# Optimization experiments

Hardware: AMD Instinct MI355X
Metric: run time of the kernel (lower is better)

## Reference

```python
import jax, jax.numpy as jnp
import numpy as np

B, S, E, H = 4, 2048, 1024, 16
HD = E // H  # head_dim = 64


def setup_inputs() -> dict:
    key = jax.random.key(0)
    k1, k2, k3, k4 = jax.random.split(key, 4)
    x = jax.random.normal(k1, (B, S, E), dtype=jnp.float32)
    Wqkv = jax.random.normal(k2, (3 * E, E), dtype=jnp.float32) * (E ** -0.5)
    Wo = jax.random.normal(k3, (E, E), dtype=jnp.float32) * (E ** -0.5)
    bo = jax.random.normal(k4, (E,), dtype=jnp.float32) * 0.01
    return {"x": x, "Wqkv": Wqkv, "Wo": Wo, "bo": bo}


def reference(x, Wqkv, Wo, bo):
    b, s, e = x.shape
    # qkv projection (nn.Linear without bias: x @ W^T) -> (b, s, 3e)
    qkv = x @ Wqkv.T
    # reshape (b, s, H, 3*HD) -> (b, H, s, 3*HD), then chunk into q,k,v
    qkv = qkv.reshape(b, s, H, 3 * HD).transpose(0, 2, 1, 3)
    q, k, v = jnp.split(qkv, 3, axis=-1)  # each (b, H, s, HD)
    scale = 1.0 / jnp.sqrt(jnp.asarray(HD, dtype=x.dtype))
    scores = jnp.einsum('bhqd,bhkd->bhqk', q, k) * scale  # (b, H, s, s)
    causal = jnp.tril(jnp.ones((s, s), dtype=bool))
    scores = jnp.where(causal, scores, -jnp.inf)
    probs = jax.nn.softmax(scores, axis=-1)
    out = jnp.einsum('bhqk,bhkd->bhqd', probs, v)  # (b, H, s, HD)
    out = out.transpose(0, 2, 1, 3).reshape(b, s, e)
    return out @ Wo.T + bo
```

## Files before the change

kernel.cpp:

```cpp
#include <hip/hip_runtime.h>
#include <stdint.h>

#define Bn 4
#define Sn 2048
#define En 1024
#define Hn 16
#define HDn 64

typedef __bf16 bf16;
typedef __bf16 bf16x4 __attribute__((ext_vector_type(4)));
typedef __bf16 bf16x8 __attribute__((ext_vector_type(8)));
typedef float  f32x4  __attribute__((ext_vector_type(4)));
typedef float  f32x16 __attribute__((ext_vector_type(16)));
typedef uint32_t u32x4 __attribute__((ext_vector_type(4)));

#define GLDS(gp, lp) __builtin_amdgcn_global_load_lds( \
    (const __attribute__((address_space(1))) void*)(gp), \
    (__attribute__((address_space(3))) void*)(lp), 16, 0, 0)

#define BAR() __builtin_amdgcn_s_barrier()
#define WLG() do { asm volatile("s_waitcnt lgkmcnt(0)" ::: "memory"); \
                   __builtin_amdgcn_sched_barrier(0); } while (0)
#define WVM4() asm volatile("s_waitcnt vmcnt(4)" ::: "memory")
#define WVM0() asm volatile("s_waitcnt vmcnt(0)" ::: "memory")

__global__ __launch_bounds__(256) void cvt_f32_to_bf16(
    const float* __restrict__ in, bf16* __restrict__ out, int n4)
{
    int i = blockIdx.x * 256 + threadIdx.x;
    if (i >= n4) return;
    float4 f = reinterpret_cast<const float4*>(in)[i];
    bf16x4 o;
    o[0] = (bf16)f.x; o[1] = (bf16)f.y; o[2] = (bf16)f.z; o[3] = (bf16)f.w;
    reinterpret_cast<bf16x4*>(out)[i] = o;
}

template<int MODE>
__global__ __launch_bounds__(512, 2) void gemm256(
    const bf16* __restrict__ Ag, const bf16* __restrict__ Bw,
    int M, int N, int K,
    bf16* __restrict__ q_out, bf16* __restrict__ k_out, bf16* __restrict__ v_out,
    float* __restrict__ c_out, const float* __restrict__ bias)
{
    __shared__ __align__(16) bf16 lA[2 * 256 * 64];
    __shared__ __align__(16) bf16 lB[2 * 256 * 64];

    const int tid  = threadIdx.x;
    const int lane = tid & 63;
    const int w    = tid >> 6;
    const int wm = w >> 2, wn = w & 3;
    const int lr = lane & 15, lg = lane >> 4;
    const int m0 = blockIdx.y * 256;
    const int n0 = blockIdx.x * 256;
    const int NT = K >> 6;
    const int niter = NT >> 1;

    const int srow = tid >> 3;
    const int sck  = (tid & 7) ^ ((tid >> 3) & 7);

    f32x4 acc[8][4] = {};

    auto stageA = [&](int t, int half) {
        const int ts = t < NT ? t : NT - 1;
        bf16* Ld = lA + ((t & 1) ? 16384 : 0) + (half*128 + w*8) * 64;
        const bf16* S = Ag + (size_t)(m0 + half*128 + srow) * K + ts*64 + sck*8;
        GLDS(S, Ld);
        GLDS(S + (size_t)64 * K, Ld + 64 * 64);
    };
    auto stageB = [&](int t, int half) {
        const int ts = t < NT ? t : NT - 1;
        bf16* Ld = lB + ((t & 1) ? 16384 : 0) + (half*128 + w*8) * 64;
        const bf16* S = Bw + (size_t)(n0 + half*128 + srow) * K + ts*64 + sck*8;
        GLDS(S, Ld);
        GLDS(S + (size_t)64 * K, Ld + 64 * 64);
    };
    auto ldA4 = [&](bf16x8 (&a)[4][2], const bf16* Lb, int qm) {
        #pragma unroll
        for (int ii = 0; ii < 4; ++ii) {
            const bf16* p = Lb + (wm*128 + qm*64 + ii*16 + lr) * 64;
            #pragma unroll
            for (int kk = 0; kk < 2; ++kk)
                a[ii][kk] = *reinterpret_cast<const bf16x8*>(p + (((kk << 2) + lg) ^ (lr & 7)) * 8);
        }
    };
    auto ldB2 = [&](bf16x8 (&b)[2][2], const bf16* Lb, int qn) {
        #pragma unroll
        for (int j = 0; j < 2; ++j) {
            const bf16* p = Lb + (wn*64 + qn*32 + j*16 + lr) * 64;
            #pragma unroll
            for (int kk = 0; kk < 2; ++kk)
                b[j][kk] = *reinterpret_cast<const bf16x8*>(p + (((kk << 2) + lg) ^ (lr & 7)) * 8);
        }
    };
    auto mmac = [&](const bf16x8 (&a)[4][2], const bf16x8 (&b)[2][2], int qm, int qn) {
        __builtin_amdgcn_s_setprio(1);
        #pragma unroll
        for (int ii = 0; ii < 4; ++ii)
            #pragma unroll
            for (int j = 0; j < 2; ++j)
                #pragma unroll
                for (int kk = 0; kk < 2; ++kk)
                    acc[qm*4 + ii][qn*2 + j] = __builtin_amdgcn_mfma_f32_16x16x32_bf16(
                        a[ii][kk], b[j][kk], acc[qm*4 + ii][qn*2 + j], 0, 0, 0);
        __builtin_amdgcn_s_setprio(0);
    };

    stageA(0, 0); stageA(0, 1); stageB(0, 0); stageB(0, 1);
    stageB(1, 0); stageB(1, 1);
    WVM4(); BAR();

    const bf16* A0 = lA;          const bf16* A1 = lA + 16384;
    const bf16* B0l = lB;         const bf16* B1l = lB + 16384;
    bf16x8 a[4][2], b0[2][2], b1[2][2];

    for (int i = 0; i < niter; ++i) {
        const int t = 2 * i;
        ldA4(a, A0, 0); ldB2(b0, B0l, 0);
        stageA(t + 1, 0);
        BAR(); WLG();
        mmac(a, b0, 0, 0);
        BAR();
        ldB2(b1, B0l, 1);
        stageA(t + 1, 1);
        BAR(); WLG();
        mmac(a, b1, 0, 1);
        BAR();
        ldA4(a, A0, 1);
        stageB(t + 2, 0);
        BAR(); WLG();
        mmac(a, b0, 1, 0);
        BAR();
        stageB(t + 2, 1);
        WVM4(); BAR();
        mmac(a, b1, 1, 1);
        BAR();
        ldA4(a, A1, 0); ldB2(b0, B1l, 0);
        stageA(t + 2, 0);
        BAR(); WLG();
        mmac(a, b0, 0, 0);
        BAR();
        ldB2(b1, B1l, 1);
        stageA(t + 2, 1);
        BAR(); WLG();
        mmac(a, b1, 0, 1);
        BAR();
        ldA4(a, A1, 1);
        stageB(t + 3, 0);
        BAR(); WLG();
        mmac(a, b0, 1, 0);
        BAR();
        stageB(t + 3, 1);
        WVM4(); BAR();
        mmac(a, b1, 1, 1);
        BAR();
    }

    #pragma unroll
    for (int ii = 0; ii < 8; ++ii) {
        #pragma unroll
        for (int j = 0; j < 4; ++j) {
            const int colb = n0 + wn*64 + j*16 + lr;
            #pragma unroll
            for (int r = 0; r < 4; ++r) {
                const int rowb = m0 + wm*128 + ii*16 + lg*4 + r;
                const float v = acc[ii][j][r];
                if (MODE == 0) {
                    const int bb = rowb >> 11, s = rowb & (Sn - 1);
                    const int h = colb / 192, rr = colb - h*192;
                    const int wq = rr >> 6, hd = rr & 63;
                    const size_t off = (((size_t)(bb*Hn + h))*Sn + s)*HDn + hd;
                    const bf16 bv = (bf16)v;
                    if (wq == 0)      q_out[off] = bv;
                    else if (wq == 1) k_out[off] = bv;
                    else              v_out[off] = bv;
                } else {
                    c_out[(size_t)rowb*N + colb] = v + bias[colb];
                }
            }
        }
    }
}

template<int MODE>
__global__ __launch_bounds__(256) void gemm_bt(
    const bf16* __restrict__ A, const bf16* __restrict__ Bw,
    int M, int N, int K,
    bf16* __restrict__ q_out, bf16* __restrict__ k_out, bf16* __restrict__ v_out,
    float* __restrict__ c_out, const float* __restrict__ bias)
{
    __shared__ bf16 lA[128*64];
    __shared__ bf16 lB[128*64];
    const int tid  = threadIdx.x;
    const int lane = tid & 63;
    const int wv   = tid >> 6;
    const int wm = wv >> 1, wn = wv & 1;
    const int m0 = blockIdx.y * 128;
    const int n0 = blockIdx.x * 128;
    const int lr = lane & 15, lg = lane >> 4;

    f32x4 acc[4][4] = {};

    const int rowA = wv*8 + (lane>>3);
    const int col8 = (lane&7)*8;

    for (int k0 = 0; k0 < K; k0 += 64) {
        #pragma unroll
        for (int c = 0; c < 4; ++c) {
            int row = c*32 + rowA;
            GLDS(A  + (size_t)(m0+row)*K + k0 + col8, lA + (c*32 + wv*8)*64);
            GLDS(Bw + (size_t)(n0+row)*K + k0 + col8, lB + (c*32 + wv*8)*64);
        }
        __syncthreads();
        #pragma unroll
        for (int kk = 0; kk < 64; kk += 32) {
            bf16x8 af[4], bfv[4];
            #pragma unroll
            for (int i = 0; i < 4; ++i)
                af[i] = *reinterpret_cast<const bf16x8*>(lA + (wm*64 + i*16 + lr)*64 + kk + lg*8);
            #pragma unroll
            for (int j = 0; j < 4; ++j)
                bfv[j] = *reinterpret_cast<const bf16x8*>(lB + (wn*64 + j*16 + lr)*64 + kk + lg*8);
            #pragma unroll
            for (int i = 0; i < 4; ++i)
                #pragma unroll
                for (int j = 0; j < 4; ++j)
                    acc[i][j] = __builtin_amdgcn_mfma_f32_16x16x32_bf16(af[i], bfv[j], acc[i][j], 0, 0, 0);
        }
        __syncthreads();
    }

    #pragma unroll
    for (int i = 0; i < 4; ++i) {
        #pragma unroll
        for (int j = 0; j < 4; ++j) {
            const int colb = n0 + wn*64 + j*16 + lr;
            #pragma unroll
            for (int r = 0; r < 4; ++r) {
                const int rowb = m0 + wm*64 + i*16 + lg*4 + r;
                const float v = acc[i][j][r];
                if (MODE == 0) {
                    const int b = rowb >> 11, s = rowb & (Sn-1);
                    const int h = colb / 192, rr = colb - h*192;
                    const int wq = rr >> 6, hd = rr & 63;
                    const size_t off = (((size_t)(b*Hn + h))*Sn + s)*HDn + hd;
                    const bf16 bv = (bf16)v;
                    if (wq == 0)      q_out[off] = bv;
                    else if (wq == 1) k_out[off] = bv;
                    else              v_out[off] = bv;
                } else {
                    c_out[(size_t)rowb*N + colb] = v + bias[colb];
                }
            }
        }
    }
}

static __device__ __forceinline__ uint32_t pkbf(float lo, float hi)
{
    uint16_t a = __builtin_bit_cast(uint16_t, (bf16)lo);
    uint16_t b = __builtin_bit_cast(uint16_t, (bf16)hi);
    return (uint32_t)a | ((uint32_t)b << 16);
}

__global__ __launch_bounds__(512) void attn_fwd(
    const bf16* __restrict__ Q, const bf16* __restrict__ Kg, const bf16* __restrict__ Vg,
    bf16* __restrict__ O)
{
    __shared__ __align__(16) bf16 Kl[2][64*64];
    __shared__ __align__(16) bf16 Vt[2][64*64];

    const int tid  = threadIdx.x;
    const int lane = tid & 63;
    const int w    = tid >> 6;
    const int col  = lane & 31;
    const int hv   = lane >> 5;
    const int bh   = blockIdx.x;
    const int qb   = (gridDim.y - 1) - blockIdx.y;
    const int q0w  = qb*256 + w*32;
    const int qg   = q0w + col;

    const bf16* Qb = Q  + (size_t)bh*Sn*HDn;
    const bf16* Kb = Kg + (size_t)bh*Sn*HDn;
    const bf16* Vb = Vg + (size_t)bh*Sn*HDn;

    bf16x8 aq[4];
    #pragma unroll
    for (int ks = 0; ks < 4; ++ks)
        aq[ks] = *reinterpret_cast<const bf16x8*>(Qb + (size_t)qg*HDn + ks*16 + hv*8);

    f32x16 ov[2] = {};
    const float S2 = 0.18033688011112042f;
    float m_run = -1e30f, l_run = 0.f;

    const int srow = tid >> 3;
    const int scol = tid & 7;
    const int ksw  = scol ^ (srow & 7);

    auto vWrite = [&](bf16* Vd, bf16x8 vv) {
        #pragma unroll
        for (int j = 0; j < 8; ++j) {
            const int chunk = (scol*8 + j)*8 + ((srow>>3) ^ scol);
            Vd[chunk*8 + (srow&7)] = vv[j];
        }
    };

    const int nkt = 4*(qb+1);

    GLDS(Kb + (size_t)srow*HDn + ksw*8, &Kl[0][0] + (size_t)w*512);
    {
        bf16x8 vv0 = *reinterpret_cast<const bf16x8*>(Vb + (size_t)srow*HDn + scol*8);
        WVM0();
        vWrite(&Vt[0][0], vv0);
    }
    __syncthreads();

    for (int kt = 0; kt < nkt; ++kt) {
        const int cur = kt & 1;
        const int k0 = kt*64;
        const bool more = (kt + 1 < nkt);
        const bool skip = (k0 > q0w + 31);

        bf16x8 vv;
        if (more) {
            GLDS(Kb + (size_t)(k0 + 64 + srow)*HDn + ksw*8, &Kl[cur^1][0] + (size_t)w*512);
            vv = *reinterpret_cast<const bf16x8*>(Vb + (size_t)(k0 + 64 + srow)*HDn + scol*8);
        }

        uint32_t wpk[2][8];
        if (!skip) {
            f32x16 st[2] = {};
            __builtin_amdgcn_s_setprio(1);
            #pragma unroll
            for (int kb = 0; kb < 2; ++kb) {
                const int key = kb*32 + col;
                #pragma unroll
                for (int ks = 0; ks < 4; ++ks) {
                    const int chunk = key*8 + ((ks*2 + hv) ^ (key & 7));
                    bf16x8 kf = *reinterpret_cast<const bf16x8*>(&Kl[cur][0] + chunk*8);
                    st[kb] = __builtin_amdgcn_mfma_f32_32x32x16_bf16(kf, aq[ks], st[kb], 0, 0, 0);
                }
            }
            __builtin_amdgcn_s_setprio(0);

            if (k0 + 63 > q0w) {
                #pragma unroll
                for (int kb = 0; kb < 2; ++kb)
                    #pragma unroll
                    for (int r = 0; r < 16; ++r) {
                        const int keyg = k0 + kb*32 + (r&3) + 8*(r>>2) + 4*hv;
                        if (keyg > qg) st[kb][r] = -1e30f;
                    }
            }

            float mx = st[0][0];
            #pragma unroll
            for (int kb = 0; kb < 2; ++kb)
                #pragma unroll
                for (int r = 0; r < 16; ++r)
                    mx = fmaxf(mx, st[kb][r]);
            mx = fmaxf(mx, __shfl_xor(mx, 32));
            const float smax2 = mx * S2;

            if (!__all(smax2 - m_run <= 8.0f)) {
                const float mn = fmaxf(m_run, smax2);
                const float fr = exp2f(m_run - mn);
                l_run *= fr;
                #pragma unroll
                for (int hb = 0; hb < 2; ++hb)
                    #pragma unroll
                    for (int r = 0; r < 16; ++r)
                        ov[hb][r] *= fr;
                m_run = mn;
            }

            float sum = 0.f;
            #pragma unroll
            for (int kb = 0; kb < 2; ++kb)
                #pragma unroll
                for (int i = 0; i < 8; ++i) {
                    const float e0 = exp2f(fmaf(st[kb][2*i],   S2, -m_run));
                    const float e1 = exp2f(fmaf(st[kb][2*i+1], S2, -m_run));
                    sum += e0 + e1;
                    wpk[kb][i] = pkbf(e0, e1);
                }
            l_run += sum;
        }

        WVM0();
        if (more) vWrite(&Vt[cur^1][0], vv);

        if (!skip) {
            #pragma unroll
            for (int s = 0; s < 4; ++s) {
                const int kb = s >> 1, ls = s & 1;
                const uint32_t send0 = hv ? wpk[kb][4*ls+0] : wpk[kb][4*ls+2];
                const uint32_t send1 = hv ? wpk[kb][4*ls+1] : wpk[kb][4*ls+3];
                const uint32_t keep0 = hv ? wpk[kb][4*ls+2] : wpk[kb][4*ls+0];
                const uint32_t keep1 = hv ? wpk[kb][4*ls+3] : wpk[kb][4*ls+1];
                const uint32_t r0 = (uint32_t)__shfl_xor((int)send0, 32);
                const uint32_t r1 = (uint32_t)__shfl_xor((int)send1, 32);
                u32x4 pwv = { hv ? r0 : keep0, hv ? r1 : keep1,
                              hv ? keep0 : r0, hv ? keep1 : r1 };
                bf16x8 pB = __builtin_bit_cast(bf16x8, pwv);
                __builtin_amdgcn_s_setprio(1);
                #pragma unroll
                for (int hb = 0; hb < 2; ++hb) {
                    const int hd = hb*32 + col;
                    const int chunk = hd*8 + ((s*2 + hv) ^ ((hd>>3) & 7));
                    bf16x8 vf = *reinterpret_cast<const bf16x8*>(&Vt[cur][0] + chunk*8);
                    ov[hb] = __builtin_amdgcn_mfma_f32_32x32x16_bf16(vf, pB, ov[hb], 0, 0, 0);
                }
                __builtin_amdgcn_s_setprio(0);
            }
        }

        __syncthreads();
    }

    const float lt  = l_run + __shfl_xor(l_run, 32);
    const float inv = 1.0f / lt;
    const int b = bh >> 4, hh = bh & 15;
    bf16* Ob = O + ((size_t)(b*Sn + qg))*En + hh*HDn;
    #pragma unroll
    for (int hb = 0; hb < 2; ++hb)
        #pragma unroll
        for (int g = 0; g < 4; ++g) {
            bf16x4 o4;
            #pragma unroll
            for (int r4 = 0; r4 < 4; ++r4)
                o4[r4] = (bf16)(ov[hb][g*4 + r4] * inv);
            *reinterpret_cast<bf16x4*>(Ob + hb*32 + g*8 + 4*hv) = o4;
        }
}

extern "C" void kernel_launch(void* const* d_in, const int* in_sizes, int n_in,
                              void* d_out, int out_size, void* d_ws, size_t ws_size,
                              hipStream_t stream)
{
    (void)in_sizes; (void)n_in; (void)out_size; (void)ws_size;
    const float* x    = (const float*)d_in[0];
    const float* Wqkv = (const float*)d_in[1];
    const float* Wo   = (const float*)d_in[2];
    const float* bo   = (const float*)d_in[3];
    float* out = (float*)d_out;

    const size_t nBS = (size_t)Bn*Sn;
    char* ws = (char*)d_ws;
    bf16* xb    = (bf16*)ws; ws += nBS*En*2;
    bf16* wqkvb = (bf16*)ws; ws += (size_t)3*En*En*2;
    bf16* wob   = (bf16*)ws; ws += (size_t)En*En*2;
    bf16* Qb    = (bf16*)ws; ws += nBS*En*2;
    bf16* Kb    = (bf16*)ws; ws += nBS*En*2;
    bf16* Vb    = (bf16*)ws; ws += nBS*En*2;
    bf16* AO    = (bf16*)ws; ws += nBS*En*2;

    int n4 = (int)(nBS*En/4);
    cvt_f32_to_bf16<<<(n4+255)/256, 256, 0, stream>>>(x, xb, n4);
    n4 = 3*En*En/4;
    cvt_f32_to_bf16<<<(n4+255)/256, 256, 0, stream>>>(Wqkv, wqkvb, n4);
    n4 = En*En/4;
    cvt_f32_to_bf16<<<(n4+255)/256, 256, 0, stream>>>(Wo, wob, n4);

    gemm256<0><<<dim3(3*En/256, nBS/256), 512, 0, stream>>>(
        xb, wqkvb, (int)nBS, 3*En, En, Qb, Kb, Vb, nullptr, nullptr);

    attn_fwd<<<dim3(Bn*Hn, Sn/256), 512, 0, stream>>>(Qb, Kb, Vb, AO);

    gemm_bt<1><<<dim3(En/128, nBS/128), 256, 0, stream>>>(
        AO, wob, (int)nBS, En, En, nullptr, nullptr, nullptr, out, bo);
}
```

Before: 204.3 us.

## Prefetch K/V tiles into registers and store to LDS after compute

The attention kernel now loads the next K tile through registers instead of global_load_lds, and writes both the K and V prefetches into the other LDS buffer only after the QK^T, softmax and PV work for the current tile. This moves the vmcnt wait to the end of the iteration so global load latency overlaps the whole compute phase. The max and sum reductions are also rewritten as trees to shorten the dependency chains. The MODE 0 epilogue is removed from gemm_bt. The trade-off is more VGPR pressure from holding the prefetched tiles in registers, and an unconditional (redundant) load on the last iteration.

```diff
diff --git a/kernel.cpp b/kernel.cpp
--- a/kernel.cpp
+++ b/kernel.cpp
@@ -185,7 +185,6 @@
 __global__ __launch_bounds__(256) void gemm_bt(
     const bf16* __restrict__ A, const bf16* __restrict__ Bw,
     int M, int N, int K,
-    bf16* __restrict__ q_out, bf16* __restrict__ k_out, bf16* __restrict__ v_out,
     float* __restrict__ c_out, const float* __restrict__ bias)
 {
     __shared__ bf16 lA[128*64];
@@ -237,19 +236,7 @@
             #pragma unroll
             for (int r = 0; r < 4; ++r) {
                 const int rowb = m0 + wm*64 + i*16 + lg*4 + r;
-                const float v = acc[i][j][r];
-                if (MODE == 0) {
-                    const int b = rowb >> 11, s = rowb & (Sn-1);
-                    const int h = colb / 192, rr = colb - h*192;
-                    const int wq = rr >> 6, hd = rr & 63;
-                    const size_t off = (((size_t)(b*Hn + h))*Sn + s)*HDn + hd;
-                    const bf16 bv = (bf16)v;
-                    if (wq == 0)      q_out[off] = bv;
-                    else if (wq == 1) k_out[off] = bv;
-                    else              v_out[off] = bv;
-                } else {
-                    c_out[(size_t)rowb*N + colb] = v + bias[colb];
-                }
+                c_out[(size_t)rowb*N + colb] = acc[i][j][r] + bias[colb];
             }
         }
     }
@@ -293,40 +280,37 @@
     float m_run = -1e30f, l_run = 0.f;
 
     const int srow = tid >> 3;
-    const int scol = tid & 7;
-    const int ksw  = scol ^ (srow & 7);
+    const int scc  = tid & 7;
+    const int koff = srow*64 + (scc ^ (srow & 7))*8;
 
     auto vWrite = [&](bf16* Vd, bf16x8 vv) {
         #pragma unroll
         for (int j = 0; j < 8; ++j) {
-            const int chunk = (scol*8 + j)*8 + ((srow>>3) ^ scol);
+            const int chunk = (scc*8 + j)*8 + ((srow>>3) ^ scc);
             Vd[chunk*8 + (srow&7)] = vv[j];
         }
     };
 
     const int nkt = 4*(qb+1);
 
-    GLDS(Kb + (size_t)srow*HDn + ksw*8, &Kl[0][0] + (size_t)w*512);
     {
-        bf16x8 vv0 = *reinterpret_cast<const bf16x8*>(Vb + (size_t)srow*HDn + scol*8);
-        WVM0();
-        vWrite(&Vt[0][0], vv0);
+        bf16x8 k0r = *reinterpret_cast<const bf16x8*>(Kb + (size_t)srow*HDn + scc*8);
+        bf16x8 v0r = *reinterpret_cast<const bf16x8*>(Vb + (size_t)srow*HDn + scc*8);
+        *reinterpret_cast<bf16x8*>(&Kl[0][koff]) = k0r;
+        vWrite(&Vt[0][0], v0r);
     }
     __syncthreads();
 
     for (int kt = 0; kt < nkt; ++kt) {
-        const int cur = kt & 1;
-        const int k0 = kt*64;
+        const int cur  = kt & 1;
+        const int k0   = kt*64;
         const bool more = (kt + 1 < nkt);
         const bool skip = (k0 > q0w + 31);
-
-        bf16x8 vv;
-        if (more) {
-            GLDS(Kb + (size_t)(k0 + 64 + srow)*HDn + ksw*8, &Kl[cur^1][0] + (size_t)w*512);
-            vv = *reinterpret_cast<const bf16x8*>(Vb + (size_t)(k0 + 64 + srow)*HDn + scol*8);
-        }
-
-        uint32_t wpk[2][8];
+        const int kn   = more ? (k0 + 64) : k0;
+
+        bf16x8 kreg = *reinterpret_cast<const bf16x8*>(Kb + (size_t)(kn + srow)*HDn + scc*8);
+        bf16x8 vreg = *reinterpret_cast<const bf16x8*>(Vb + (size_t)(kn + srow)*HDn + scc*8);
+
         if (!skip) {
             f32x16 st[2] = {};
             __builtin_amdgcn_s_setprio(1);
@@ -335,8 +319,8 @@
                 const int key = kb*32 + col;
                 #pragma unroll
                 for (int ks = 0; ks < 4; ++ks) {
-                    const int chunk = key*8 + ((ks*2 + hv) ^ (key & 7));
-                    bf16x8 kf = *reinterpret_cast<const bf16x8*>(&Kl[cur][0] + chunk*8);
+                    const int slot = (ks*2 + hv) ^ (key & 7);
+                    bf16x8 kf = *reinterpret_cast<const bf16x8*>(&Kl[cur][0] + key*64 + slot*8);
                     st[kb] = __builtin_amdgcn_mfma_f32_32x32x16_bf16(kf, aq[ks], st[kb], 0, 0, 0);
                 }
             }
@@ -352,13 +336,16 @@
                     }
             }
 
-            float mx = st[0][0];
-            #pragma unroll
-            for (int kb = 0; kb < 2; ++kb)
-                #pragma unroll
-                for (int r = 0; r < 16; ++r)
-                    mx = fmaxf(mx, st[kb][r]);
-            mx = fmaxf(mx, __shfl_xor(mx, 32));
+            float m16[8];
+            #pragma unroll
+            for (int r = 0; r < 8; ++r)
+                m16[r] = fmaxf(fmaxf(st[0][r], st[0][r+8]), fmaxf(st[1][r], st[1][r+8]));
+            #pragma unroll
+            for (int d = 4; d; d >>= 1)
+                #pragma unroll
+                for (int r = 0; r < d; ++r)
+                    m16[r] = fmaxf(m16[r], m16[r+d]);
+            float mx = fmaxf(m16[0], __shfl_xor(m16[0], 32));
             const float smax2 = mx * S2;
 
             if (!__all(smax2 - m_run <= 8.0f)) {
@@ -373,23 +360,24 @@
                 m_run = mn;
             }
 
-            float sum = 0.f;
-            #pragma unroll
-            for (int kb = 0; kb < 2; ++kb)
+            uint32_t wpk[2][8];
+            float lsum = 0.f;
+            #pragma unroll
+            for (int kb = 0; kb < 2; ++kb) {
+                float pr[8];
                 #pragma unroll
                 for (int i = 0; i < 8; ++i) {
                     const float e0 = exp2f(fmaf(st[kb][2*i],   S2, -m_run));
                     const float e1 = exp2f(fmaf(st[kb][2*i+1], S2, -m_run));
-                    sum += e0 + e1;
+                    pr[i] = e0 + e1;
                     wpk[kb][i] = pkbf(e0, e1);
                 }
-            l_run += sum;
-        }
-
-        WVM0();
-        if (more) vWrite(&Vt[cur^1][0], vv);
-
-        if (!skip) {
+                pr[0] += pr[4]; pr[1] += pr[5]; pr[2] += pr[6]; pr[3] += pr[7];
+                pr[0] += pr[2]; pr[1] += pr[3];
+                lsum += pr[0] + pr[1];
+            }
+            l_run += lsum;
+
             #pragma unroll
             for (int s = 0; s < 4; ++s) {
                 const int kb = s >> 1, ls = s & 1;
@@ -406,14 +394,19 @@
                 #pragma unroll
                 for (int hb = 0; hb < 2; ++hb) {
                     const int hd = hb*32 + col;
-                    const int chunk = hd*8 + ((s*2 + hv) ^ ((hd>>3) & 7));
-                    bf16x8 vf = *reinterpret_cast<const bf16x8*>(&Vt[cur][0] + chunk*8);
+                    const int slot = (s*2 + hv) ^ ((hd>>3) & 7);
+                    bf16x8 vf = *reinterpret_cast<const bf16x8*>(&Vt[cur][0] + hd*64 + slot*8);
                     ov[hb] = __builtin_amdgcn_mfma_f32_32x32x16_bf16(vf, pB, ov[hb], 0, 0, 0);
                 }
                 __builtin_amdgcn_s_setprio(0);
             }
         }
 
+        WVM0();
+        if (more) {
+            *reinterpret_cast<bf16x8*>(&Kl[cur^1][koff]) = kreg;
+            vWrite(&Vt[cur^1][0], vreg);
+        }
         __syncthreads();
     }
 
@@ -467,5 +460,5 @@
     attn_fwd<<<dim3(Bn*Hn, Sn/256), 512, 0, stream>>>(Qb, Kb, Vb, AO);
 
     gemm_bt<1><<<dim3(En/128, nBS/128), 256, 0, stream>>>(
-        AO, wob, (int)nBS, En, En, nullptr, nullptr, nullptr, out, bo);
-}
+        AO, wob, (int)nBS, En, En, out, bo);
+}
```

Result: no change. 202.4 us (-0.9%).
